# Kernel optimization log

Hardware: AMD Instinct MI355X
Metric: run time of the kernel (lower is better)

Reference implementation:

```python
import jax, jax.numpy as jnp
import numpy as np

B, N, D = 16, 1024, 128


def setup_inputs() -> dict:
    key = jax.random.key(0)
    ks = jax.random.split(key, 12)
    x = jax.random.normal(ks[0], (B, N, D), dtype=jnp.float32)
    # binary symmetric-ish adjacency mask (0/1 floats)
    adj = jax.random.randint(ks[1], (B, N, N), 0, 2).astype(jnp.float32)
    Ww = jax.random.normal(ks[2], (D, D), dtype=jnp.float32) * 0.05
    Wb = jax.random.normal(ks[3], (D,), dtype=jnp.float32) * 0.05
    A = jax.random.normal(ks[4], (D, D), dtype=jnp.float32) * 0.05
    wi_u = jax.random.normal(ks[5], (D,), dtype=jnp.float32) * 0.05
    wi_x = jax.random.normal(ks[6], (D,), dtype=jnp.float32) * 0.05
    wf_u = jax.random.normal(ks[7], (D,), dtype=jnp.float32) * 0.05
    wf_x = jax.random.normal(ks[8], (D,), dtype=jnp.float32) * 0.05
    wo_u = jax.random.normal(ks[9], (D,), dtype=jnp.float32) * 0.05
    wo_x = jax.random.normal(ks[10], (D,), dtype=jnp.float32) * 0.05
    return {"x": x, "adj": adj, "Ww": Ww, "Wb": Wb, "A": A,
            "wi_u": wi_u, "wi_x": wi_x, "wf_u": wf_u, "wf_x": wf_x,
            "wo_u": wo_u, "wo_x": wo_x}


def reference(x, adj, Ww, Wb, A, wi_u, wi_x, wf_u, wf_x, wo_u, wo_x):
    # h = W(x): [B,N,D]
    h = jnp.einsum('bnf,df->bnd', x, Ww) + Wb
    # e[b,j,k] = (h A) . h  -> symmetrized dense scores [B,N,N]
    e = jnp.einsum('bjl,bkl->bjk', jnp.einsum('bjd,dl->bjl', h, A), h)
    e = e + jnp.swapaxes(e, 1, 2)
    # masked softmax over axis=1 (columns), then re-mask by adj
    scores = jnp.where(adj > 0, e, 0.0)
    attention = jax.nn.softmax(scores, axis=1) * adj
    # aggregation
    h_prime = jax.nn.relu(jnp.einsum('bij,bjk->bik', attention, h))
    # LSTM-style gates: scalar per node, broadcast over features
    ic = jax.nn.sigmoid(h_prime @ wi_u + x @ wi_x)[..., None]
    fc = jax.nn.sigmoid(h_prime @ wf_u + x @ wf_x)[..., None]
    oc = jax.nn.sigmoid(h_prime @ wo_u + x @ wo_x)[..., None]
    return oc * jnp.tanh(ic * h_prime + fc * x)
```

## Files before the change

### kernel.cpp

```cpp
#include <hip/hip_runtime.h>


#define B_ 16
#define N_ 1024
#define D_ 128

typedef __attribute__((ext_vector_type(8))) short bf16x8;
typedef __attribute__((ext_vector_type(4))) float f32x4;

__device__ __forceinline__ float b2f(unsigned short u) {
    union { unsigned int i; float f; } v; v.i = ((unsigned int)u) << 16; return v.f;
}
__device__ __forceinline__ unsigned short f2b(float f) {
    union { float f; unsigned int i; } v; v.f = f;
    unsigned int x = v.i;
    return (unsigned short)((x + 0x7fffu + ((x >> 16) & 1u)) >> 16);
}
__device__ __forceinline__ float clamp60(float v) {
    return fminf(fmaxf(v, -60.f), 60.f);
}
__device__ __forceinline__ bf16x8 load8f(const float* p) {
    float4 a = *reinterpret_cast<const float4*>(p);
    float4 b = *reinterpret_cast<const float4*>(p + 4);
    bf16x8 v;
    v[0] = (short)f2b(a.x); v[1] = (short)f2b(a.y);
    v[2] = (short)f2b(a.z); v[3] = (short)f2b(a.w);
    v[4] = (short)f2b(b.x); v[5] = (short)f2b(b.y);
    v[6] = (short)f2b(b.z); v[7] = (short)f2b(b.w);
    return v;
}

__global__ __launch_bounds__(256) void k0_w2t(
    const float* __restrict__ Ww, const float* __restrict__ Wb,
    const float* __restrict__ A, unsigned short* __restrict__ WwB,
    unsigned short* __restrict__ W2T, float* __restrict__ wbA) {
    int t = blockIdx.x * 256 + threadIdx.x;
    int l = t >> 7, f = t & 127;
    float acc = 0.f;
    for (int d = 0; d < 128; ++d)
        acc += A[d * 128 + l] * Ww[d * 128 + f];
    W2T[l * 128 + f] = f2b(acc);
    WwB[t] = f2b(Ww[t]);
    if (blockIdx.x == 0 && threadIdx.x < 128) {
        float s = 0.f;
        for (int d = 0; d < 128; ++d) s += Wb[d] * A[d * 128 + threadIdx.x];
        wbA[threadIdx.x] = s;
    }
}

__global__ __launch_bounds__(256) void kmask(
    const float* __restrict__ adj, unsigned long long* __restrict__ maskJ) {
    int w = threadIdx.x >> 6, lane = threadIdx.x & 63;
    size_t base = ((size_t)blockIdx.x * 4 + w) * 256;
    unsigned long long w0 = __ballot(adj[base + 0 * 64 + lane] > 0.f);
    unsigned long long w1 = __ballot(adj[base + 1 * 64 + lane] > 0.f);
    unsigned long long w2 = __ballot(adj[base + 2 * 64 + lane] > 0.f);
    unsigned long long w3 = __ballot(adj[base + 3 * 64 + lane] > 0.f);
    unsigned long long o = lane == 0 ? w0 : lane == 1 ? w1 : lane == 2 ? w2 : w3;
    if (lane < 4) maskJ[(base >> 6) + lane] = o;
}

__global__ __launch_bounds__(256) void k1_hu(
    const float* __restrict__ x, const unsigned short* __restrict__ WwB,
    const float* __restrict__ Wb, const unsigned short* __restrict__ W2T,
    const float* __restrict__ wbA,
    unsigned short* __restrict__ h, unsigned short* __restrict__ u,
    unsigned short* __restrict__ hT) {
    __shared__ unsigned short lds[16][128];
    int w = threadIdx.x >> 6, lane = threadIdx.x & 63;
    int c = lane & 15, q = lane >> 4;
    int rowbase = blockIdx.x * 16;
    int b = rowbase >> 10;
    int n0 = rowbase & 1023;
    bf16x8 xa[4];
    const float* xrow = x + (size_t)(rowbase + c) * 128;
#pragma unroll
    for (int ks = 0; ks < 4; ++ks)
        xa[ks] = load8f(xrow + ks * 32 + q * 8);
#pragma unroll
    for (int tt = 0; tt < 2; ++tt) {
        int t = w * 2 + tt;
        f32x4 acch = {0.f, 0.f, 0.f, 0.f};
        f32x4 accu = {0.f, 0.f, 0.f, 0.f};
        const unsigned short* wwrow = WwB + (t * 16 + c) * 128;
        const unsigned short* w2row = W2T + (t * 16 + c) * 128;
#pragma unroll
        for (int ks = 0; ks < 4; ++ks) {
            bf16x8 bw = *reinterpret_cast<const bf16x8*>(wwrow + ks * 32 + q * 8);
            bf16x8 b2 = *reinterpret_cast<const bf16x8*>(w2row + ks * 32 + q * 8);
            acch = __builtin_amdgcn_mfma_f32_16x16x32_bf16(xa[ks], bw, acch, 0, 0, 0);
            accu = __builtin_amdgcn_mfma_f32_16x16x32_bf16(xa[ks], b2, accu, 0, 0, 0);
        }
        float wb = Wb[t * 16 + c];
        float ub = wbA[t * 16 + c];
#pragma unroll
        for (int r = 0; r < 4; ++r) {
            int row = rowbase + q * 4 + r;
            unsigned short hv = f2b(acch[r] + wb);
            unsigned short uv = f2b(accu[r] + ub);
            h[(size_t)row * 128 + t * 16 + c] = hv;
            u[(size_t)row * 128 + t * 16 + c] = uv;
            lds[q * 4 + r][t * 16 + c] = hv;
        }
    }
    __syncthreads();
    int tid = threadIdx.x;
    if (tid < 128) {
        int d = tid;
        unsigned int p[8];
#pragma unroll
        for (int k = 0; k < 8; ++k) {
            unsigned int v0 = lds[2 * k][d], v1 = lds[2 * k + 1][d];
            p[k] = v0 | (v1 << 16);
        }
        size_t basehT = ((size_t)(b * 128 + d)) * 1024 + n0;
        uint4* dst = reinterpret_cast<uint4*>(hT + basehT);
        dst[0] = make_uint4(p[0], p[1], p[2], p[3]);
        dst[1] = make_uint4(p[4], p[5], p[6], p[7]);
    }
}

__global__ __launch_bounds__(256) void k2_scores(
    const unsigned short* __restrict__ h, const unsigned short* __restrict__ u,
    const unsigned long long* __restrict__ maskJ,
    unsigned short* __restrict__ att, float* __restrict__ colpart) {
    __shared__ unsigned long long lmask[32][16];
    __shared__ __align__(16) unsigned short stage[4][32][40];
    int w = threadIdx.x >> 6, lane = threadIdx.x & 63;
    int c = lane & 15, q = lane >> 4;
    int b = blockIdx.x >> 5;
    int iblk = blockIdx.x & 31;
    int i0 = iblk * 32;
    const unsigned short* hb = h + (size_t)b * N_ * D_;
    const unsigned short* ub = u + (size_t)b * N_ * D_;

    {
        int tid = threadIdx.x;
        lmask[tid >> 4][tid & 15] =
            maskJ[(size_t)(b * 1024 + i0 + (tid >> 4)) * 16 + (tid & 15)];
        lmask[16 + (tid >> 4)][tid & 15] =
            maskJ[(size_t)(b * 1024 + i0 + 16 + (tid >> 4)) * 16 + (tid & 15)];
    }
    __syncthreads();

    bf16x8 Au0[4], Ah0[4], Au1[4], Ah1[4];
#pragma unroll
    for (int ks = 0; ks < 4; ++ks) {
        Au0[ks] = *reinterpret_cast<const bf16x8*>(ub + (i0 + c) * 128 + ks * 32 + q * 8);
        Ah0[ks] = *reinterpret_cast<const bf16x8*>(hb + (i0 + c) * 128 + ks * 32 + q * 8);
        Au1[ks] = *reinterpret_cast<const bf16x8*>(ub + (i0 + 16 + c) * 128 + ks * 32 + q * 8);
        Ah1[ks] = *reinterpret_cast<const bf16x8*>(hb + (i0 + 16 + c) * 128 + ks * 32 + q * 8);
    }
    unsigned short* attrow = att + ((size_t)(b * 1024 + i0)) * 1024;
    float* cprow = colpart + ((size_t)(b * 32 + iblk)) * 1024;

    int jt0 = w * 16;
#pragma unroll
    for (int p = 0; p < 8; ++p) {
        int jt = jt0 + p * 2;
        int j0 = jt * 16;
        bf16x8 Bh[2][4], Bu[2][4];
#pragma unroll
        for (int s = 0; s < 2; ++s)
#pragma unroll
            for (int ks = 0; ks < 4; ++ks) {
                Bh[s][ks] = *reinterpret_cast<const bf16x8*>(
                    hb + (j0 + s * 16 + c) * 128 + ks * 32 + q * 8);
                Bu[s][ks] = *reinterpret_cast<const bf16x8*>(
                    ub + (j0 + s * 16 + c) * 128 + ks * 32 + q * 8);
            }
        f32x4 acc[2][2][2];
#pragma unroll
        for (int g = 0; g < 2; ++g)
#pragma unroll
            for (int s = 0; s < 2; ++s)
#pragma unroll
                for (int pr = 0; pr < 2; ++pr)
                    acc[g][s][pr] = (f32x4){0.f, 0.f, 0.f, 0.f};
#pragma unroll
        for (int ks = 0; ks < 4; ++ks) {
            acc[0][0][0] = __builtin_amdgcn_mfma_f32_16x16x32_bf16(Au0[ks], Bh[0][ks], acc[0][0][0], 0, 0, 0);
            acc[0][0][1] = __builtin_amdgcn_mfma_f32_16x16x32_bf16(Ah0[ks], Bu[0][ks], acc[0][0][1], 0, 0, 0);
            acc[1][0][0] = __builtin_amdgcn_mfma_f32_16x16x32_bf16(Au1[ks], Bh[0][ks], acc[1][0][0], 0, 0, 0);
            acc[1][0][1] = __builtin_amdgcn_mfma_f32_16x16x32_bf16(Ah1[ks], Bu[0][ks], acc[1][0][1], 0, 0, 0);
            acc[0][1][0] = __builtin_amdgcn_mfma_f32_16x16x32_bf16(Au0[ks], Bh[1][ks], acc[0][1][0], 0, 0, 0);
            acc[0][1][1] = __builtin_amdgcn_mfma_f32_16x16x32_bf16(Ah0[ks], Bu[1][ks], acc[0][1][1], 0, 0, 0);
            acc[1][1][0] = __builtin_amdgcn_mfma_f32_16x16x32_bf16(Au1[ks], Bh[1][ks], acc[1][1][0], 0, 0, 0);
            acc[1][1][1] = __builtin_amdgcn_mfma_f32_16x16x32_bf16(Ah1[ks], Bu[1][ks], acc[1][1][1], 0, 0, 0);
        }
        float colpA = 0.f, colpB = 0.f;
#pragma unroll
        for (int s = 0; s < 2; ++s) {
            int jts = jt + s;
            int wd = jts >> 2, sh = (jts & 3) * 16;
#pragma unroll
            for (int g = 0; g < 2; ++g)
#pragma unroll
                for (int r = 0; r < 4; ++r) {
                    float e = acc[g][s][0][r] + acc[g][s][1][r];
                    int row = g * 16 + q * 4 + r;
                    bool m = (lmask[row][wd] >> (sh + c)) & 1ull;
                    float ex = m ? __expf(clamp60(e)) : 0.f;
                    float cadd = m ? ex : 1.0f;
                    if (s == 0) colpA += cadd; else colpB += cadd;
                    stage[w][row][s * 16 + c] = f2b(ex);
                }
        }
        colpA += __shfl_xor(colpA, 16, 64);
        colpA += __shfl_xor(colpA, 32, 64);
        colpB += __shfl_xor(colpB, 16, 64);
        colpB += __shfl_xor(colpB, 32, 64);
        if (q == 0) {
            cprow[j0 + c] = colpA;
            cprow[j0 + 16 + c] = colpB;
        }
        int row2 = lane & 31, half = lane >> 5;
        const uint4* sp = reinterpret_cast<const uint4*>(&stage[w][row2][half * 16]);
        uint4 v0 = sp[0], v1 = sp[1];
        uint4* gp = reinterpret_cast<uint4*>(attrow + (size_t)row2 * 1024 + j0 + half * 16);
        gp[0] = v0; gp[1] = v1;
    }
}

__global__ __launch_bounds__(256) void k2b_recip(
    const float* __restrict__ colpart, float* __restrict__ rl0) {
    int g = blockIdx.x * 256 + threadIdx.x;
    int b = g >> 10, j = g & 1023;
    float s = 0.f;
    const float* p = colpart + (size_t)b * 32 * 1024 + j;
    for (int ib = 0; ib < 32; ++ib) s += p[(size_t)ib * 1024];
    rl0[g] = 1.0f / s;
}

__global__ __launch_bounds__(256) void k3_gemm(
    const unsigned short* __restrict__ att, const float* __restrict__ rl0,
    const unsigned short* __restrict__ hT, const float* __restrict__ x,
    const float* __restrict__ wi_u, const float* __restrict__ wi_x,
    const float* __restrict__ wf_u, const float* __restrict__ wf_x,
    const float* __restrict__ wo_u, const float* __restrict__ wo_x,
    float* __restrict__ out) {
    __shared__ float red[4][16][129];
    int w = threadIdx.x >> 6, lane = threadIdx.x & 63;
    int c = lane & 15, q = lane >> 4;
    int b = blockIdx.x >> 6;
    int i0 = (blockIdx.x & 63) * 16;
    const unsigned short* attrow = att + ((size_t)(b * 1024 + i0 + c)) * 1024;
    const unsigned short* hTb = hT + (size_t)b * 128 * 1024;
    const float* rl0b = rl0 + b * 1024;
    f32x4 hp[8];
#pragma unroll
    for (int t = 0; t < 8; ++t) hp[t] = (f32x4){0.f, 0.f, 0.f, 0.f};
#pragma unroll
    for (int tt = 0; tt < 8; ++tt) {
        int jp = w * 8 + tt;
        int jb = jp * 32 + q * 8;
        bf16x8 eraw = *reinterpret_cast<const bf16x8*>(attrow + jb);
        float4 r0 = *reinterpret_cast<const float4*>(rl0b + jb);
        float4 r1 = *reinterpret_cast<const float4*>(rl0b + jb + 4);
        bf16x8 av;
        av[0] = (short)f2b(b2f((unsigned short)eraw[0]) * r0.x);
        av[1] = (short)f2b(b2f((unsigned short)eraw[1]) * r0.y);
        av[2] = (short)f2b(b2f((unsigned short)eraw[2]) * r0.z);
        av[3] = (short)f2b(b2f((unsigned short)eraw[3]) * r0.w);
        av[4] = (short)f2b(b2f((unsigned short)eraw[4]) * r1.x);
        av[5] = (short)f2b(b2f((unsigned short)eraw[5]) * r1.y);
        av[6] = (short)f2b(b2f((unsigned short)eraw[6]) * r1.z);
        av[7] = (short)f2b(b2f((unsigned short)eraw[7]) * r1.w);
#pragma unroll
        for (int t = 0; t < 8; ++t) {
            bf16x8 bt = *reinterpret_cast<const bf16x8*>(
                hTb + (size_t)(t * 16 + c) * 1024 + jp * 32 + q * 8);
            hp[t] = __builtin_amdgcn_mfma_f32_16x16x32_bf16(av, bt, hp[t], 0, 0, 0);
        }
    }
#pragma unroll
    for (int t = 0; t < 8; ++t)
#pragma unroll
        for (int r = 0; r < 4; ++r)
            red[w][q * 4 + r][t * 16 + c] = hp[t][r];
    __syncthreads();
    if (w != 0) return;
#pragma unroll
    for (int t = 0; t < 8; ++t)
#pragma unroll
        for (int r = 0; r < 4; ++r)
            hp[t][r] = red[0][q * 4 + r][t * 16 + c] + red[1][q * 4 + r][t * 16 + c]
                     + red[2][q * 4 + r][t * 16 + c] + red[3][q * 4 + r][t * 16 + c];
    float xv[8][4];
#pragma unroll
    for (int t = 0; t < 8; ++t)
#pragma unroll
        for (int r = 0; r < 4; ++r) {
            hp[t][r] = fmaxf(hp[t][r], 0.f);
            xv[t][r] = x[(size_t)(b * 1024 + i0 + q * 4 + r) * 128 + t * 16 + c];
        }
    float wiu[8], wix[8], wfu[8], wfx[8], wou[8], wox[8];
#pragma unroll
    for (int t = 0; t < 8; ++t) {
        wiu[t] = wi_u[t * 16 + c]; wix[t] = wi_x[t * 16 + c];
        wfu[t] = wf_u[t * 16 + c]; wfx[t] = wf_x[t * 16 + c];
        wou[t] = wo_u[t * 16 + c]; wox[t] = wo_x[t * 16 + c];
    }
#pragma unroll
    for (int r = 0; r < 4; ++r) {
        float zi = 0.f, zf = 0.f, zo = 0.f;
#pragma unroll
        for (int t = 0; t < 8; ++t) {
            zi += hp[t][r] * wiu[t] + xv[t][r] * wix[t];
            zf += hp[t][r] * wfu[t] + xv[t][r] * wfx[t];
            zo += hp[t][r] * wou[t] + xv[t][r] * wox[t];
        }
        zi += __shfl_xor(zi, 1, 64); zi += __shfl_xor(zi, 2, 64);
        zi += __shfl_xor(zi, 4, 64); zi += __shfl_xor(zi, 8, 64);
        zf += __shfl_xor(zf, 1, 64); zf += __shfl_xor(zf, 2, 64);
        zf += __shfl_xor(zf, 4, 64); zf += __shfl_xor(zf, 8, 64);
        zo += __shfl_xor(zo, 1, 64); zo += __shfl_xor(zo, 2, 64);
        zo += __shfl_xor(zo, 4, 64); zo += __shfl_xor(zo, 8, 64);
        float ic = 1.f / (1.f + __expf(-zi));
        float fc = 1.f / (1.f + __expf(-zf));
        float oc = 1.f / (1.f + __expf(-zo));
#pragma unroll
        for (int t = 0; t < 8; ++t) {
            float zz = ic * hp[t][r] + fc * xv[t][r];
            float th = 1.f - 2.f / (__expf(2.f * zz) + 1.f);
            out[(size_t)(b * 1024 + i0 + q * 4 + r) * 128 + t * 16 + c] = oc * th;
        }
    }
}

extern "C" void kernel_launch(void* const* d_in, const int* in_sizes, int n_in,
                              void* d_out, int out_size, void* d_ws, size_t ws_size,
                              hipStream_t stream) {
    const float* x    = (const float*)d_in[0];
    const float* adj  = (const float*)d_in[1];
    const float* Ww   = (const float*)d_in[2];
    const float* Wb   = (const float*)d_in[3];
    const float* A    = (const float*)d_in[4];
    const float* wi_u = (const float*)d_in[5];
    const float* wi_x = (const float*)d_in[6];
    const float* wf_u = (const float*)d_in[7];
    const float* wf_x = (const float*)d_in[8];
    const float* wo_u = (const float*)d_in[9];
    const float* wo_x = (const float*)d_in[10];
    float* out = (float*)d_out;
    char* ws = (char*)d_ws;

    if (ws_size >= (56ull << 20)) {
        unsigned short* WwB = (unsigned short*)(ws);
        unsigned short* W2T = (unsigned short*)(ws + (32u << 10));
        float* wbA          = (float*)(ws + (64u << 10));
        float* rl0          = (float*)(ws + (128u << 10));
        unsigned long long* maskJ = (unsigned long long*)(ws + (256u << 10));
        float* colpart      = (float*)(ws + (4ull << 20));
        unsigned short* h   = (unsigned short*)(ws + (8ull << 20));
        unsigned short* u   = (unsigned short*)(ws + (12ull << 20));
        unsigned short* hT  = (unsigned short*)(ws + (16ull << 20));
        unsigned short* att = (unsigned short*)(ws + (20ull << 20));

        k0_w2t<<<64, 256, 0, stream>>>(Ww, Wb, A, WwB, W2T, wbA);
        kmask<<<16384, 256, 0, stream>>>(adj, maskJ);
        k1_hu<<<1024, 256, 0, stream>>>(x, WwB, Wb, W2T, wbA, h, u, hT);
        k2_scores<<<512, 256, 0, stream>>>(h, u, maskJ, att, colpart);
        k2b_recip<<<64, 256, 0, stream>>>(colpart, rl0);
        k3_gemm<<<1024, 256, 0, stream>>>(att, rl0, hT, x,
                                          wi_u, wi_x, wf_u, wf_x, wo_u, wo_x, out);
    } else {
        unsigned short* WwB = (unsigned short*)(ws);
        unsigned short* W2T = (unsigned short*)(ws + (32u << 10));
        float* wbA          = (float*)(ws + (64u << 10));
        float* rl0          = (float*)(ws + (128u << 10));
        unsigned long long* maskJ = (unsigned long long*)(ws + (256u << 10));
        float* colpart      = (float*)(ws + (3ull << 20));
        unsigned short* h   = (unsigned short*)(ws + (5ull << 20));
        unsigned short* u   = (unsigned short*)(ws + (9ull << 20));
        unsigned short* hT  = (unsigned short*)(ws + (13ull << 20));
        unsigned short* att = (unsigned short*)(ws + (17ull << 20));

        k0_w2t<<<64, 256, 0, stream>>>(Ww, Wb, A, WwB, W2T, wbA);
        kmask<<<16384, 256, 0, stream>>>(adj, maskJ);
        k1_hu<<<1024, 256, 0, stream>>>(x, WwB, Wb, W2T, wbA, h, u, hT);
        k2_scores<<<512, 256, 0, stream>>>(h, u, maskJ, att, colpart);
        k2b_recip<<<64, 256, 0, stream>>>(colpart, rl0);
        k3_gemm<<<1024, 256, 0, stream>>>(att, rl0, hT, x,
                                          wi_u, wi_x, wf_u, wf_x, wo_u, wo_x, out);
    }
}
```

Baseline: 224.2 us.

## Split k3 GEMM across waves by output columns with LDS-staged attention tile

The aggregation kernel used to split the reduction dimension across four waves. That forced a large LDS reduction, after which only one wave ran the gate epilogue. Now each wave owns two 16-column output tiles over the full K=1024. The 16x1024 attention tile is staged once into swizzled LDS via global_load_lds so all waves share it. Gate dot products are reduced with a small LDS exchange, so all waves run the epilogue, at the cost of longer serial MFMA chains per wave.

```diff
diff --git a/kernel.cpp b/kernel.cpp
--- a/kernel.cpp
+++ b/kernel.cpp
@@ -239,24 +239,44 @@
     const float* __restrict__ wf_u, const float* __restrict__ wf_x,
     const float* __restrict__ wo_u, const float* __restrict__ wo_x,
     float* __restrict__ out) {
-    __shared__ float red[4][16][129];
+    __shared__ __align__(16) unsigned short smem[16384];
     int w = threadIdx.x >> 6, lane = threadIdx.x & 63;
     int c = lane & 15, q = lane >> 4;
     int b = blockIdx.x >> 6;
     int i0 = (blockIdx.x & 63) * 16;
-    const unsigned short* attrow = att + ((size_t)(b * 1024 + i0 + c)) * 1024;
+
+    const char* attblk = reinterpret_cast<const char*>(att + ((size_t)(b * 1024 + i0)) * 1024);
+#pragma unroll
+    for (int it = 0; it < 8; ++it) {
+        int L = it * 4096 + w * 1024;
+        int row = L >> 11;
+        int swz = (row & 7) << 4;
+        int cb = (L & 2047) + lane * 16;
+        const char* src = attblk + (row << 11) + (cb ^ swz);
+        unsigned short* dst = smem + (L >> 1);
+        __builtin_amdgcn_global_load_lds(
+            (const __attribute__((address_space(1))) unsigned int*)(const void*)src,
+            (__attribute__((address_space(3))) unsigned int*)(void*)dst, 16, 0, 0);
+    }
+    __syncthreads();
+
+    int t0 = w * 2, t1 = t0 + 1;
     const unsigned short* hTb = hT + (size_t)b * 128 * 1024;
-    const float* rl0b = rl0 + b * 1024;
-    f32x4 hp[8];
-#pragma unroll
-    for (int t = 0; t < 8; ++t) hp[t] = (f32x4){0.f, 0.f, 0.f, 0.f};
-#pragma unroll
-    for (int tt = 0; tt < 8; ++tt) {
-        int jp = w * 8 + tt;
-        int jb = jp * 32 + q * 8;
-        bf16x8 eraw = *reinterpret_cast<const bf16x8*>(attrow + jb);
-        float4 r0 = *reinterpret_cast<const float4*>(rl0b + jb);
-        float4 r1 = *reinterpret_cast<const float4*>(rl0b + jb + 4);
+    const unsigned short* bt0p = hTb + (size_t)(t0 * 16 + c) * 1024 + q * 8;
+    const unsigned short* bt1p = hTb + (size_t)(t1 * 16 + c) * 1024 + q * 8;
+    const float* rl0p = rl0 + b * 1024 + q * 8;
+    const char* avbase = reinterpret_cast<const char*>(smem) + c * 2048;
+    int swzc = (c & 7) << 4;
+    int offq = q * 16;
+
+    f32x4 acc0 = {0.f, 0.f, 0.f, 0.f};
+    f32x4 acc1 = {0.f, 0.f, 0.f, 0.f};
+#pragma unroll 4
+    for (int jp = 0; jp < 32; ++jp) {
+        bf16x8 eraw = *reinterpret_cast<const bf16x8*>(
+            avbase + (((jp << 6) + offq) ^ swzc));
+        float4 r0 = *reinterpret_cast<const float4*>(rl0p + jp * 32);
+        float4 r1 = *reinterpret_cast<const float4*>(rl0p + jp * 32 + 4);
         bf16x8 av;
         av[0] = (short)f2b(b2f((unsigned short)eraw[0]) * r0.x);
         av[1] = (short)f2b(b2f((unsigned short)eraw[1]) * r0.y);
@@ -266,64 +286,74 @@
         av[5] = (short)f2b(b2f((unsigned short)eraw[5]) * r1.y);
         av[6] = (short)f2b(b2f((unsigned short)eraw[6]) * r1.z);
         av[7] = (short)f2b(b2f((unsigned short)eraw[7]) * r1.w);
-#pragma unroll
-        for (int t = 0; t < 8; ++t) {
-            bf16x8 bt = *reinterpret_cast<const bf16x8*>(
-                hTb + (size_t)(t * 16 + c) * 1024 + jp * 32 + q * 8);
-            hp[t] = __builtin_amdgcn_mfma_f32_16x16x32_bf16(av, bt, hp[t], 0, 0, 0);
-        }
-    }
-#pragma unroll
-    for (int t = 0; t < 8; ++t)
-#pragma unroll
-        for (int r = 0; r < 4; ++r)
-            red[w][q * 4 + r][t * 16 + c] = hp[t][r];
+        bf16x8 b0 = *reinterpret_cast<const bf16x8*>(bt0p + jp * 32);
+        bf16x8 b1 = *reinterpret_cast<const bf16x8*>(bt1p + jp * 32);
+        acc0 = __builtin_amdgcn_mfma_f32_16x16x32_bf16(av, b0, acc0, 0, 0, 0);
+        acc1 = __builtin_amdgcn_mfma_f32_16x16x32_bf16(av, b1, acc1, 0, 0, 0);
+    }
+
+    float hp[2][4], xv[2][4];
+    const float* xb = x + ((size_t)(b * 1024 + i0)) * 128;
+#pragma unroll
+    for (int r = 0; r < 4; ++r) {
+        hp[0][r] = fmaxf(acc0[r], 0.f);
+        hp[1][r] = fmaxf(acc1[r], 0.f);
+        xv[0][r] = xb[(size_t)(q * 4 + r) * 128 + t0 * 16 + c];
+        xv[1][r] = xb[(size_t)(q * 4 + r) * 128 + t1 * 16 + c];
+    }
+    float wiu[2], wix[2], wfu[2], wfx[2], wou[2], wox[2];
+#pragma unroll
+    for (int tt = 0; tt < 2; ++tt) {
+        int d = (t0 + tt) * 16 + c;
+        wiu[tt] = wi_u[d]; wix[tt] = wi_x[d];
+        wfu[tt] = wf_u[d]; wfx[tt] = wf_x[d];
+        wou[tt] = wo_u[d]; wox[tt] = wo_x[d];
+    }
+    float zi[4], zf[4], zo[4];
+#pragma unroll
+    for (int r = 0; r < 4; ++r) {
+        zi[r] = hp[0][r] * wiu[0] + hp[1][r] * wiu[1]
+              + xv[0][r] * wix[0] + xv[1][r] * wix[1];
+        zf[r] = hp[0][r] * wfu[0] + hp[1][r] * wfu[1]
+              + xv[0][r] * wfx[0] + xv[1][r] * wfx[1];
+        zo[r] = hp[0][r] * wou[0] + hp[1][r] * wou[1]
+              + xv[0][r] * wox[0] + xv[1][r] * wox[1];
+        zi[r] += __shfl_xor(zi[r], 1, 64); zi[r] += __shfl_xor(zi[r], 2, 64);
+        zi[r] += __shfl_xor(zi[r], 4, 64); zi[r] += __shfl_xor(zi[r], 8, 64);
+        zf[r] += __shfl_xor(zf[r], 1, 64); zf[r] += __shfl_xor(zf[r], 2, 64);
+        zf[r] += __shfl_xor(zf[r], 4, 64); zf[r] += __shfl_xor(zf[r], 8, 64);
+        zo[r] += __shfl_xor(zo[r], 1, 64); zo[r] += __shfl_xor(zo[r], 2, 64);
+        zo[r] += __shfl_xor(zo[r], 4, 64); zo[r] += __shfl_xor(zo[r], 8, 64);
+    }
     __syncthreads();
-    if (w != 0) return;
-#pragma unroll
-    for (int t = 0; t < 8; ++t)
-#pragma unroll
-        for (int r = 0; r < 4; ++r)
-            hp[t][r] = red[0][q * 4 + r][t * 16 + c] + red[1][q * 4 + r][t * 16 + c]
-                     + red[2][q * 4 + r][t * 16 + c] + red[3][q * 4 + r][t * 16 + c];
-    float xv[8][4];
-#pragma unroll
-    for (int t = 0; t < 8; ++t)
+    float* gp = reinterpret_cast<float*>(smem);
+    if (c == 0) {
 #pragma unroll
         for (int r = 0; r < 4; ++r) {
-            hp[t][r] = fmaxf(hp[t][r], 0.f);
-            xv[t][r] = x[(size_t)(b * 1024 + i0 + q * 4 + r) * 128 + t * 16 + c];
-        }
-    float wiu[8], wix[8], wfu[8], wfx[8], wou[8], wox[8];
-#pragma unroll
-    for (int t = 0; t < 8; ++t) {
-        wiu[t] = wi_u[t * 16 + c]; wix[t] = wi_x[t * 16 + c];
-        wfu[t] = wf_u[t * 16 + c]; wfx[t] = wf_x[t * 16 + c];
-        wou[t] = wo_u[t * 16 + c]; wox[t] = wo_x[t * 16 + c];
-    }
+            int row = q * 4 + r;
+            gp[(w * 16 + row) * 4 + 0] = zi[r];
+            gp[(w * 16 + row) * 4 + 1] = zf[r];
+            gp[(w * 16 + row) * 4 + 2] = zo[r];
+        }
+    }
+    __syncthreads();
 #pragma unroll
     for (int r = 0; r < 4; ++r) {
-        float zi = 0.f, zf = 0.f, zo = 0.f;
-#pragma unroll
-        for (int t = 0; t < 8; ++t) {
-            zi += hp[t][r] * wiu[t] + xv[t][r] * wix[t];
-            zf += hp[t][r] * wfu[t] + xv[t][r] * wfx[t];
-            zo += hp[t][r] * wou[t] + xv[t][r] * wox[t];
-        }
-        zi += __shfl_xor(zi, 1, 64); zi += __shfl_xor(zi, 2, 64);
-        zi += __shfl_xor(zi, 4, 64); zi += __shfl_xor(zi, 8, 64);
-        zf += __shfl_xor(zf, 1, 64); zf += __shfl_xor(zf, 2, 64);
-        zf += __shfl_xor(zf, 4, 64); zf += __shfl_xor(zf, 8, 64);
-        zo += __shfl_xor(zo, 1, 64); zo += __shfl_xor(zo, 2, 64);
-        zo += __shfl_xor(zo, 4, 64); zo += __shfl_xor(zo, 8, 64);
-        float ic = 1.f / (1.f + __expf(-zi));
-        float fc = 1.f / (1.f + __expf(-zf));
-        float oc = 1.f / (1.f + __expf(-zo));
-#pragma unroll
-        for (int t = 0; t < 8; ++t) {
-            float zz = ic * hp[t][r] + fc * xv[t][r];
+        int row = q * 4 + r;
+        float Zi = gp[(0 * 16 + row) * 4 + 0] + gp[(1 * 16 + row) * 4 + 0]
+                 + gp[(2 * 16 + row) * 4 + 0] + gp[(3 * 16 + row) * 4 + 0];
+        float Zf = gp[(0 * 16 + row) * 4 + 1] + gp[(1 * 16 + row) * 4 + 1]
+                 + gp[(2 * 16 + row) * 4 + 1] + gp[(3 * 16 + row) * 4 + 1];
+        float Zo = gp[(0 * 16 + row) * 4 + 2] + gp[(1 * 16 + row) * 4 + 2]
+                 + gp[(2 * 16 + row) * 4 + 2] + gp[(3 * 16 + row) * 4 + 2];
+        float ic = 1.f / (1.f + __expf(-Zi));
+        float fc = 1.f / (1.f + __expf(-Zf));
+        float oc = 1.f / (1.f + __expf(-Zo));
+#pragma unroll
+        for (int tt = 0; tt < 2; ++tt) {
+            float zz = ic * hp[tt][r] + fc * xv[tt][r];
             float th = 1.f - 2.f / (__expf(2.f * zz) + 1.f);
-            out[(size_t)(b * 1024 + i0 + q * 4 + r) * 128 + t * 16 + c] = oc * th;
+            out[(size_t)(b * 1024 + i0 + row) * 128 + (t0 + tt) * 16 + c] = oc * th;
         }
     }
 }
```

Result: no change. 225.2 us (+0.4%).
